# Kernel tuning notes

Hardware: AMD Instinct MI355X
Metric: run time of the kernel (lower is better)

Reference implementation:

```python
import jax, jax.numpy as jnp
import numpy as np

B = 16384          # batch
IN = 256           # input_dim
HID = [1024, 1024, 512]
K = 8              # num_mixtures
D = 16             # latent_dim
NT = D * (D + 1) // 2  # 136 packed tril components per mixture

_rows, _cols = np.tril_indices(D)          # row-major lower-tri order, same as nested loops
_rows = jnp.asarray(_rows); _cols = jnp.asarray(_cols)
_diag_mask = _rows == _cols                # [NT] bool


def setup_inputs() -> dict:
    key = jax.random.key(0)
    ks = jax.random.split(key, 12)

    def lin(k, fi, fo):
        kw, kb = jax.random.split(k)
        s = 1.0 / np.sqrt(fi)
        W = (jax.random.uniform(kw, (fi, fo), minval=-s, maxval=s)).astype(jnp.float32)
        b = (jax.random.uniform(kb, (fo,), minval=-s, maxval=s)).astype(jnp.float32)
        return W, b

    W0, b0 = lin(ks[0], IN, HID[0])
    W1, b1 = lin(ks[1], HID[0], HID[1])
    W2, b2 = lin(ks[2], HID[1], HID[2])
    Wpi, bpi = lin(ks[3], HID[2], K)
    Wmu, bmu = lin(ks[4], HID[2], K * D)
    Wt, bt = lin(ks[5], HID[2], K * NT)
    x = jax.random.normal(ks[6], (B, IN), dtype=jnp.float32)
    return dict(x=x, W0=W0, b0=b0, W1=W1, b1=b1, W2=W2, b2=b2,
                Wpi=Wpi, bpi=bpi, Wmu=Wmu, bmu=bmu, Wt=Wt, bt=bt)


def reference(x, W0, b0, W1, b1, W2, b2, Wpi, bpi, Wmu, bmu, Wt, bt):
    # MLP trunk: Linear + ReLU chain
    h = jax.nn.relu(x @ W0 + b0)
    h = jax.nn.relu(h @ W1 + b1)
    h = jax.nn.relu(h @ W2 + b2)
    # Heads
    pi_k = jax.nn.softmax(h @ Wpi + bpi, axis=1)                 # [B, K]
    mu_k = (h @ Wmu + bmu).reshape(-1, K, D)                     # [B, K, D]
    tc = (h @ Wt + bt).reshape(-1, K, NT)                        # [B, K, NT]
    # Fused cholesky-tril assembly: exp on diagonal entries, copy off-diagonal,
    # scattered into lower triangle in row-major (i, j<=i) order.
    vals = jnp.where(_diag_mask, jnp.exp(tc), tc)                # [B, K, NT]
    tril = jnp.zeros((tc.shape[0], K, D, D), dtype=tc.dtype)
    tril = tril.at[:, :, _rows, _cols].set(vals)                 # [B, K, D, D]
    return pi_k, mu_k, tril
```

## Files before the change

### kernel.cpp

```cpp
#include <hip/hip_runtime.h>
#include <hip/hip_bf16.h>
#include <cstdint>
#include <cstddef>

typedef __attribute__((ext_vector_type(8))) _Float16 half8;
typedef __attribute__((ext_vector_type(4))) float f32x4;
typedef __attribute__((ext_vector_type(8))) unsigned short ushort8v;
typedef __attribute__((ext_vector_type(4))) unsigned short ushort4v;

__device__ __forceinline__ unsigned short f2h_bits(float x) {
  _Float16 h = (_Float16)x;
  union { _Float16 h; unsigned short u; } cv; cv.h = h; return cv.u;
}


__global__ __launch_bounds__(256) void k_f32_to_f16(const float* __restrict__ src,
                                                    unsigned short* __restrict__ dst, int n4) {
  int i = blockIdx.x * 256 + threadIdx.x;
  if (i >= n4) return;
  float4 v = ((const float4*)src)[i];
  ushort4v o;
  o[0] = f2h_bits(v.x); o[1] = f2h_bits(v.y); o[2] = f2h_bits(v.z); o[3] = f2h_bits(v.w);
  ((ushort4v*)dst)[i] = o;
}

__global__ __launch_bounds__(256) void k_transpose_f16(const float* __restrict__ W,
                                                       unsigned short* __restrict__ Wt,
                                                       int Kd, int N) {
  int tid = blockIdx.x * 256 + threadIdx.x;
  int total = (Kd >> 3) * N;
  if (tid >= total) return;
  int kc = tid / N;
  int n  = tid - kc * N;
  int k0 = kc << 3;
  ushort8v o;
#pragma unroll
  for (int j = 0; j < 8; ++j) o[j] = f2h_bits(W[(size_t)(k0 + j) * N + n]);
  *(ushort8v*)(&Wt[(size_t)n * Kd + k0]) = o;
}

__global__ __launch_bounds__(256) void k_build_head(
    const float* __restrict__ Wmu, const float* __restrict__ Wt,
    const float* __restrict__ Wpi,
    const float* __restrict__ bmu, const float* __restrict__ bt,
    const float* __restrict__ bpi,
    unsigned short* __restrict__ whd, float* __restrict__ bhd)
{
  int tid = blockIdx.x * 256 + threadIdx.x;
  if (tid >= 2304 * 64) return;
  int r  = tid >> 6;
  int d0 = (tid & 63) << 3;

  const float* src = nullptr; int stride = 0;
  if (r < 128) { src = Wmu + r; stride = 128; }
  else if (r < 2176) {
    int rU = r - 128, k = rU >> 8, i = (rU >> 4) & 15, j = rU & 15;
    if (j <= i) { src = Wt + k * 136 + ((i * (i + 1)) >> 1) + j; stride = 1088; }
  } else if (r < 2184) { src = Wpi + (r - 2176); stride = 8; }

  ushort8v o;
#pragma unroll
  for (int jj = 0; jj < 8; ++jj)
    o[jj] = src ? f2h_bits(src[(size_t)(d0 + jj) * stride]) : (unsigned short)0;
  *(ushort8v*)(&whd[(size_t)r * 512 + d0]) = o;

  if (d0 == 0) {
    float b = 0.f;
    if (r < 128) b = bmu[r];
    else if (r < 2176) {
      int rU = r - 128, k = rU >> 8, i = (rU >> 4) & 15, j = rU & 15;
      if (j <= i) b = bt[k * 136 + ((i * (i + 1)) >> 1) + j];
    } else if (r < 2184) b = bpi[r - 2176];
    bhd[r] = b;
  }
}


template<int EPI>
__global__ __launch_bounds__(256) void k_gemm128(
    const unsigned short* __restrict__ A,
    const unsigned short* __restrict__ Bt,
    int Kd, int N,
    const float* __restrict__ bias,
    unsigned short* __restrict__ Hout,
    float* __restrict__ out_pi,
    float* __restrict__ out_mu,
    float* __restrict__ out_tril)
{
  __shared__ unsigned short Alds[2][128 * 32];
  __shared__ unsigned short Blds[2][128 * 32];

  const int tid  = threadIdx.x;
  const int lane = tid & 63;
  const int wv   = tid >> 6;
  const int wr   = wv >> 1;
  const int wc   = wv & 1;
  const int bm   = blockIdx.x << 7;
  const int bn   = blockIdx.y << 7;

  f32x4 acc[4][4] = {};

  const int l15  = lane & 15;
  const int lk   = lane >> 4;
  const int srow = lane >> 2;
  const int scol = (lane & 3) << 3;

  const unsigned short* aBase = A  + (size_t)bm * Kd;
  const unsigned short* bBase = Bt + (size_t)bn * Kd;

  auto stage = [&](int bb, int k0) {
#pragma unroll
    for (int c = 0; c < 2; ++c) {
      const int chunk = (wv << 1) + c;
      const int row = (chunk << 4) + srow;
      __builtin_amdgcn_global_load_lds(
          (const __attribute__((address_space(1))) void*)(aBase + (size_t)row * Kd + k0 + scol),
          (__attribute__((address_space(3))) void*)(&Alds[bb][chunk << 9]),
          16, 0, 0);
      __builtin_amdgcn_global_load_lds(
          (const __attribute__((address_space(1))) void*)(bBase + (size_t)row * Kd + k0 + scol),
          (__attribute__((address_space(3))) void*)(&Blds[bb][chunk << 9]),
          16, 0, 0);
    }
  };

  const int nk = Kd >> 5;
  stage(0, 0);
  __syncthreads();
  int cur = 0;
  for (int kt = 0; kt < nk; ++kt) {
    if (kt + 1 < nk) stage(cur ^ 1, (kt + 1) << 5);

    const unsigned short* al = &Alds[cur][((wr << 6) + l15) * 32 + (lk << 3)];
    const unsigned short* bl = &Blds[cur][((wc << 6) + l15) * 32 + (lk << 3)];
    half8 af[4], bfr[4];
#pragma unroll
    for (int m = 0; m < 4; ++m) af[m]  = *(const half8*)(al + (m << 9));
#pragma unroll
    for (int n = 0; n < 4; ++n) bfr[n] = *(const half8*)(bl + (n << 9));
#pragma unroll
    for (int m = 0; m < 4; ++m)
#pragma unroll
      for (int n = 0; n < 4; ++n)
        acc[m][n] = __builtin_amdgcn_mfma_f32_16x16x32_f16(af[m], bfr[n], acc[m][n], 0, 0, 0);

    __syncthreads();
    cur ^= 1;
  }

  const int orow = bm + (wr << 6) + (lk << 2);
#pragma unroll
  for (int m = 0; m < 4; ++m) {
#pragma unroll
    for (int n = 0; n < 4; ++n) {
      const int col = bn + (wc << 6) + (n << 4) + l15;
#pragma unroll
      for (int r = 0; r < 4; ++r) {
        const int row = orow + (m << 4) + r;
        if (EPI == 0) {
          float v = acc[m][n][r] + bias[col];
          v = v > 0.f ? v : 0.f;
          Hout[(size_t)row * N + col] = f2h_bits(v);
        } else {
          float v = acc[m][n][r] + bias[col];
          if (col < 128) {
            out_mu[(size_t)row * 128 + col] = v;
          } else if (col < 2176) {
            const int cc = col - 128;
            if (((cc >> 4) & 15) == (cc & 15)) v = expf(v);
            out_tril[(size_t)row * 2048 + cc] = v;
          } else if (col < 2184) {
            float mx = v;
#pragma unroll
            for (int s = 1; s < 8; s <<= 1) mx = fmaxf(mx, __shfl_xor(mx, s));
            float e = expf(v - mx);
            float sm = e;
#pragma unroll
            for (int s = 1; s < 8; s <<= 1) sm += __shfl_xor(sm, s);
            out_pi[((size_t)row << 3) + (col - 2176)] = e / sm;
          }
        }
      }
    }
  }
}


extern "C" void kernel_launch(void* const* d_in, const int* in_sizes, int n_in,
                              void* d_out, int out_size, void* d_ws, size_t ws_size,
                              hipStream_t stream)
{
  const float* x   = (const float*)d_in[0];
  const float* W0  = (const float*)d_in[1];
  const float* b0  = (const float*)d_in[2];
  const float* W1  = (const float*)d_in[3];
  const float* b1  = (const float*)d_in[4];
  const float* W2  = (const float*)d_in[5];
  const float* b2  = (const float*)d_in[6];
  const float* Wpi = (const float*)d_in[7];
  const float* bpi = (const float*)d_in[8];
  const float* Wmu = (const float*)d_in[9];
  const float* bmu = (const float*)d_in[10];
  const float* Wt  = (const float*)d_in[11];
  const float* bt  = (const float*)d_in[12];

  char* ws = (char*)d_ws;
  unsigned short* xh  = (unsigned short*)(ws);
  unsigned short* h0  = (unsigned short*)(ws + 8388608);
  unsigned short* h1  = (unsigned short*)(ws + 41943040);
  unsigned short* h2  = (unsigned short*)(ws + 8388608);
  unsigned short* w0b = (unsigned short*)(ws + 75497472);
  unsigned short* w1b = (unsigned short*)(ws + 76021760);
  unsigned short* w2b = (unsigned short*)(ws + 78118912);
  unsigned short* whd = (unsigned short*)(ws + 79167488);
  float*          bhd = (float*)         (ws + 81526784);

  float* out_pi   = (float*)d_out;
  float* out_mu   = (float*)d_out + 131072;
  float* out_tril = (float*)d_out + 2228224;

  k_f32_to_f16<<<4096, 256, 0, stream>>>(x, xh, 1048576);
  k_transpose_f16<<<128, 256, 0, stream>>>(W0, w0b, 256, 1024);
  k_transpose_f16<<<512, 256, 0, stream>>>(W1, w1b, 1024, 1024);
  k_transpose_f16<<<256, 256, 0, stream>>>(W2, w2b, 1024, 512);
  k_build_head<<<576, 256, 0, stream>>>(Wmu, Wt, Wpi, bmu, bt, bpi, whd, bhd);

  k_gemm128<0><<<dim3(128, 8),  256, 0, stream>>>(xh, w0b, 256, 1024, b0, h0,
                                                  nullptr, nullptr, nullptr);
  k_gemm128<0><<<dim3(128, 8),  256, 0, stream>>>(h0, w1b, 1024, 1024, b1, h1,
                                                  nullptr, nullptr, nullptr);
  k_gemm128<0><<<dim3(128, 4),  256, 0, stream>>>(h1, w2b, 1024, 512, b2, h2,
                                                  nullptr, nullptr, nullptr);
  k_gemm128<1><<<dim3(128, 18), 256, 0, stream>>>(h2, whd, 512, 2304, bhd, nullptr,
                                                  out_pi, out_mu, out_tril);
}
```

Measured before the change: 191.3 us.

## Use larger 256x256 GEMM tiles with BK=64, 8 waves and XCD-aware block swizzle

Turns the fixed 128x128 GEMM into a templated kernel with 256-wide tiles, a K step of 64 and 512 threads (8 waves in a 2x4 grid). It also adds a block-index swizzle that groups tiles across the 8 XCDs for better L2 reuse. Larger tiles raise arithmetic intensity and halve the number of K iterations and barriers. In exchange, LDS use rises to 128KB per block for 256x256, and there are more accumulator registers and fewer blocks per layer. That can hurt occupancy or leave the 256 CUs underused on the smaller GEMMs.

```diff
diff --git a/kernel.cpp b/kernel.cpp
--- a/kernel.cpp
+++ b/kernel.cpp
@@ -76,87 +76,104 @@
 }
 
 
-template<int EPI>
-__global__ __launch_bounds__(256) void k_gemm128(
+template<int BM, int BN, int EPI>
+__global__ __launch_bounds__(512, 2) void k_gemm(
     const unsigned short* __restrict__ A,
     const unsigned short* __restrict__ Bt,
-    int Kd, int N,
+    int Kd, int N, int nMb,
     const float* __restrict__ bias,
     unsigned short* __restrict__ Hout,
     float* __restrict__ out_pi,
     float* __restrict__ out_mu,
     float* __restrict__ out_tril)
 {
-  __shared__ unsigned short Alds[2][128 * 32];
-  __shared__ unsigned short Blds[2][128 * 32];
+  constexpr int BK    = 64;
+  constexpr int M_rep = BM / 32;
+  constexpr int N_rep = BN / 64;
+  constexpr int ACH   = BM / 64;
+  constexpr int BCH   = BN / 64;
+
+  __shared__ unsigned short Alds[2][BM * BK];
+  __shared__ unsigned short Blds[2][BN * BK];
 
   const int tid  = threadIdx.x;
   const int lane = tid & 63;
-  const int wv   = tid >> 6;
-  const int wr   = wv >> 1;
-  const int wc   = wv & 1;
-  const int bm   = blockIdx.x << 7;
-  const int bn   = blockIdx.y << 7;
-
-  f32x4 acc[4][4] = {};
-
+  const int wid  = tid >> 6;
+  const int wm   = wid >> 2;
+  const int wn   = wid & 3;
   const int l15  = lane & 15;
   const int lk   = lane >> 4;
-  const int srow = lane >> 2;
-  const int scol = (lane & 3) << 3;
+
+  const int cpx = gridDim.x >> 3;
+  const int bid = blockIdx.x;
+  const int swz = (bid & 7) * cpx + (bid >> 3);
+  const int bm  = (swz % nMb) * BM;
+  const int bn  = (swz / nMb) * BN;
 
   const unsigned short* aBase = A  + (size_t)bm * Kd;
   const unsigned short* bBase = Bt + (size_t)bn * Kd;
 
+  f32x4 acc[M_rep][N_rep] = {};
+
   auto stage = [&](int bb, int k0) {
 #pragma unroll
-    for (int c = 0; c < 2; ++c) {
-      const int chunk = (wv << 1) + c;
-      const int row = (chunk << 4) + srow;
+    for (int i = 0; i < ACH; ++i) {
+      const int c   = tid + (i << 9);
+      const int row = c >> 3;
+      const int col = (c & 7) << 3;
       __builtin_amdgcn_global_load_lds(
-          (const __attribute__((address_space(1))) void*)(aBase + (size_t)row * Kd + k0 + scol),
-          (__attribute__((address_space(3))) void*)(&Alds[bb][chunk << 9]),
+          (const __attribute__((address_space(1))) void*)(aBase + (size_t)row * Kd + k0 + col),
+          (__attribute__((address_space(3))) void*)(&Alds[bb][(size_t)c << 3]),
           16, 0, 0);
+    }
+#pragma unroll
+    for (int i = 0; i < BCH; ++i) {
+      const int c   = tid + (i << 9);
+      const int row = c >> 3;
+      const int col = (c & 7) << 3;
       __builtin_amdgcn_global_load_lds(
-          (const __attribute__((address_space(1))) void*)(bBase + (size_t)row * Kd + k0 + scol),
-          (__attribute__((address_space(3))) void*)(&Blds[bb][chunk << 9]),
+          (const __attribute__((address_space(1))) void*)(bBase + (size_t)row * Kd + k0 + col),
+          (__attribute__((address_space(3))) void*)(&Blds[bb][(size_t)c << 3]),
           16, 0, 0);
     }
   };
 
-  const int nk = Kd >> 5;
+  const int nk = Kd >> 6;
   stage(0, 0);
   __syncthreads();
   int cur = 0;
   for (int kt = 0; kt < nk; ++kt) {
-    if (kt + 1 < nk) stage(cur ^ 1, (kt + 1) << 5);
-
-    const unsigned short* al = &Alds[cur][((wr << 6) + l15) * 32 + (lk << 3)];
-    const unsigned short* bl = &Blds[cur][((wc << 6) + l15) * 32 + (lk << 3)];
-    half8 af[4], bfr[4];
-#pragma unroll
-    for (int m = 0; m < 4; ++m) af[m]  = *(const half8*)(al + (m << 9));
-#pragma unroll
-    for (int n = 0; n < 4; ++n) bfr[n] = *(const half8*)(bl + (n << 9));
-#pragma unroll
-    for (int m = 0; m < 4; ++m)
-#pragma unroll
-      for (int n = 0; n < 4; ++n)
-        acc[m][n] = __builtin_amdgcn_mfma_f32_16x16x32_f16(af[m], bfr[n], acc[m][n], 0, 0, 0);
+    if (kt + 1 < nk) stage(cur ^ 1, (kt + 1) << 6);
+
+    const unsigned short* al = &Alds[cur][(size_t)(wm * (BM / 2) + l15) * BK + (lk << 3)];
+    const unsigned short* bl = &Blds[cur][(size_t)(wn * (BN / 4) + l15) * BK + (lk << 3)];
+#pragma unroll
+    for (int kk = 0; kk < 2; ++kk) {
+      half8 af[M_rep], bfr[N_rep];
+#pragma unroll
+      for (int m = 0; m < M_rep; ++m) af[m]  = *(const half8*)(al + m * 16 * BK + kk * 32);
+#pragma unroll
+      for (int n = 0; n < N_rep; ++n) bfr[n] = *(const half8*)(bl + n * 16 * BK + kk * 32);
+#pragma unroll
+      for (int m = 0; m < M_rep; ++m)
+#pragma unroll
+        for (int n = 0; n < N_rep; ++n)
+          acc[m][n] = __builtin_amdgcn_mfma_f32_16x16x32_f16(af[m], bfr[n], acc[m][n], 0, 0, 0);
+    }
 
     __syncthreads();
     cur ^= 1;
   }
 
-  const int orow = bm + (wr << 6) + (lk << 2);
-#pragma unroll
-  for (int m = 0; m < 4; ++m) {
-#pragma unroll
-    for (int n = 0; n < 4; ++n) {
-      const int col = bn + (wc << 6) + (n << 4) + l15;
+  const int orow0 = bm + wm * (BM / 2) + (lk << 2);
+#pragma unroll
+  for (int m = 0; m < M_rep; ++m) {
+#pragma unroll
+    for (int n = 0; n < N_rep; ++n) {
+      const int col = bn + wn * (BN / 4) + (n << 4) + l15;
 #pragma unroll
       for (int r = 0; r < 4; ++r) {
-        const int row = orow + (m << 4) + r;
+        const int row = orow0 + (m << 4) + r;
         if (EPI == 0) {
           float v = acc[m][n][r] + bias[col];
           v = v > 0.f ? v : 0.f;
@@ -225,12 +242,12 @@
   k_transpose_f16<<<256, 256, 0, stream>>>(W2, w2b, 1024, 512);
   k_build_head<<<576, 256, 0, stream>>>(Wmu, Wt, Wpi, bmu, bt, bpi, whd, bhd);
 
-  k_gemm128<0><<<dim3(128, 8),  256, 0, stream>>>(xh, w0b, 256, 1024, b0, h0,
-                                                  nullptr, nullptr, nullptr);
-  k_gemm128<0><<<dim3(128, 8),  256, 0, stream>>>(h0, w1b, 1024, 1024, b1, h1,
-                                                  nullptr, nullptr, nullptr);
-  k_gemm128<0><<<dim3(128, 4),  256, 0, stream>>>(h1, w2b, 1024, 512, b2, h2,
-                                                  nullptr, nullptr, nullptr);
-  k_gemm128<1><<<dim3(128, 18), 256, 0, stream>>>(h2, whd, 512, 2304, bhd, nullptr,
-                                                  out_pi, out_mu, out_tril);
-}
+  k_gemm<256, 256, 0><<<256, 512, 0, stream>>>(xh, w0b, 256, 1024, 64, b0, h0,
+                                               nullptr, nullptr, nullptr);
+  k_gemm<256, 256, 0><<<256, 512, 0, stream>>>(h0, w1b, 1024, 1024, 64, b1, h1,
+                                               nullptr, nullptr, nullptr);
+  k_gemm<128, 256, 0><<<256, 512, 0, stream>>>(h1, w2b, 1024, 512, 128, b2, h2,
+                                               nullptr, nullptr, nullptr);
+  k_gemm<256, 256, 1><<<576, 512, 0, stream>>>(h2, whd, 512, 2304, 64, bhd, nullptr,
+                                               out_pi, out_mu, out_tril);
+}
```

After: 257.6 us. 1.35x slower.
